# Kernel tuning notes

Measured on AMD Instinct MI355X. Metric: run time of the kernel, lower is better.

Reference implementation:

```python
import jax, jax.numpy as jnp
import numpy as np
import math

N = 100000   # nodes
E = 1600000  # edges
D = 128      # embed_dim
H = 8        # nhead
HD = D // H  # head dim
EPS = 1e-16  # matches torch_geometric-style segment softmax eps


def _xavier(key, shape):
    fan_out, fan_in = shape
    lim = math.sqrt(6.0 / (fan_in + fan_out))
    return jax.random.uniform(key, shape, jnp.float32, -lim, lim)


def setup_inputs() -> dict:
    key = jax.random.key(0)
    ks = jax.random.split(key, 8)
    return {
        "feats": jax.random.normal(ks[0], (N, D), jnp.float32),
        "edge_index": jax.random.randint(ks[1], (E, 2), 0, N, dtype=jnp.int64),
        "edge_attr": jax.random.normal(ks[2], (E, 1), jnp.float32),
        "Wq": _xavier(ks[3], (D, D)), "bq": jnp.zeros((D,), jnp.float32),
        "Wk": _xavier(ks[4], (D, D)), "bk": jnp.zeros((D,), jnp.float32),
        "Wv": _xavier(ks[5], (D, D)), "bv": jnp.zeros((D,), jnp.float32),
        "Wo": _xavier(ks[6], (D, D)), "bo": jnp.zeros((D,), jnp.float32),
    }


def reference(feats, edge_index, edge_attr, Wq, bq, Wk, bk, Wv, bv, Wo, bo):
    # feats: [N, D]; edge_index: [E, 2] with r=src, c=dst; edge_attr unused (mult_attr=0)
    n = feats.shape[0]
    q = (feats @ Wq.T + bq).reshape(n, H, HD)  # [N, H, hd]
    k = (feats @ Wk.T + bk).reshape(n, H, HD)
    v = (feats @ Wv.T + bv).reshape(n, H, HD)

    r = edge_index[:, 0]
    c = edge_index[:, 1]

    # per-edge dot-product scores: q[dst] . k[src]
    scores = jnp.einsum('ehd,ehd->eh', q[c], k[r]) / math.sqrt(HD)  # [E, H]

    # segment softmax over edges grouped by destination node c
    smax = jax.ops.segment_max(scores, c, num_segments=n)  # [N, H]
    ex = jnp.exp(scores - smax[c])
    ssum = jax.ops.segment_sum(ex, c, num_segments=n)      # [N, H]
    alpha = ex / (ssum[c] + EPS)                           # [E, H]
    # (dropout is identity at eval time; mult_attr=0 so edge_attr unused)

    # weighted scatter-aggregate of values into destination nodes
    out = jax.ops.segment_sum(alpha[:, :, None] * v[r], c, num_segments=n)  # [N, H, hd]
    out = out.reshape(n, D) @ Wo.T + bo
    return out
```

## Files before the change

### kernel.cpp

```cpp
#include <hip/hip_runtime.h>
#include <hip/hip_bf16.h>

typedef __attribute__((ext_vector_type(8))) short bh8;
typedef __attribute__((ext_vector_type(4))) float f32x4;

__device__ __forceinline__ float bfbits2f(unsigned short s) {
    union { unsigned int u; float f; } cv;
    cv.u = ((unsigned int)s) << 16;
    return cv.f;
}
__device__ __forceinline__ unsigned short f2bfbits(float f) {
    union { float f; unsigned int u; } cv; cv.f = f;
    unsigned int u = cv.u;
    u += 0x7fffu + ((u >> 16) & 1u);
    return (unsigned short)(u >> 16);
}
__device__ __forceinline__ unsigned int pack2bf(float a, float b) {
    return (unsigned int)f2bfbits(a) | (((unsigned int)f2bfbits(b)) << 16);
}

__device__ __forceinline__ bh8 load_frag_f32(const float* __restrict__ p) {
    float4 f0 = *reinterpret_cast<const float4*>(p);
    float4 f1 = *reinterpret_cast<const float4*>(p + 4);
    bh8 r;
    r[0] = (short)f2bfbits(f0.x); r[1] = (short)f2bfbits(f0.y);
    r[2] = (short)f2bfbits(f0.z); r[3] = (short)f2bfbits(f0.w);
    r[4] = (short)f2bfbits(f1.x); r[5] = (short)f2bfbits(f1.y);
    r[6] = (short)f2bfbits(f1.z); r[7] = (short)f2bfbits(f1.w);
    return r;
}

__global__ __launch_bounds__(256)
void wconv_kernel(const float* __restrict__ w0, const float* __restrict__ w1,
                  const float* __restrict__ w2, const float* __restrict__ w3,
                  unsigned short* __restrict__ o0, unsigned short* __restrict__ o1,
                  unsigned short* __restrict__ o2, unsigned short* __restrict__ o3)
{
    const float* src[4] = {w0, w1, w2, w3};
    unsigned short* dst[4] = {o0, o1, o2, o3};
    const float* s = src[blockIdx.y];
    unsigned short* d = dst[blockIdx.y];
    int i = (blockIdx.x * 256 + threadIdx.x) * 4;
    float4 f = *reinterpret_cast<const float4*>(&s[i]);
    uint2 p;
    p.x = pack2bf(f.x, f.y);
    p.y = pack2bf(f.z, f.w);
    *reinterpret_cast<uint2*>(&d[i]) = p;
}

__global__ __launch_bounds__(256)
void qkv_scatter(const float* __restrict__ A,
                 const unsigned short* __restrict__ Wqb, const float* __restrict__ bq,
                 const unsigned short* __restrict__ Wkb, const float* __restrict__ bk,
                 const unsigned short* __restrict__ Wvb, const float* __restrict__ bv,
                 unsigned short* __restrict__ Oq, unsigned short* __restrict__ Ok,
                 unsigned short* __restrict__ Ov, int M, int gx,
                 const int* __restrict__ ei, const int* __restrict__ offsets,
                 const int* __restrict__ rank, int* __restrict__ sorted_r,
                 int E, int nsb)
{
    if (blockIdx.x >= (unsigned)gx) {
        int sb = blockIdx.x - gx;
        int stride = nsb * 256;
        for (int e = sb * 256 + threadIdx.x; e < E; e += stride) {
            int2 rc = reinterpret_cast<const int2*>(ei)[e];
            sorted_r[offsets[rc.y] + rank[e]] = rc.x;
        }
        return;
    }

    const int lane = threadIdx.x & 63;
    const int w    = threadIdx.x >> 6;
    const int r0   = blockIdx.x * 128 + w * 32;
    const int lr   = lane & 15;
    const int lk   = (lane >> 4) * 8;
    const int cq   = (lane >> 4) * 4;

    bh8 a[2][4];
    #pragma unroll
    for (int jt = 0; jt < 2; jt++) {
        int row = r0 + jt * 16 + lr; if (row >= M) row = M - 1;
        const float* ap = &A[(size_t)row * 128 + lk];
        #pragma unroll
        for (int ks = 0; ks < 4; ks++) a[jt][ks] = load_frag_f32(ap + ks * 32);
    }

    const unsigned short* Ws[3] = {Wqb, Wkb, Wvb};
    const float* Bs[3] = {bq, bk, bv};
    unsigned short* Os[3] = {Oq, Ok, Ov};

    #pragma unroll
    for (int wsel = 0; wsel < 3; wsel++) {
        const unsigned short* W = Ws[wsel];
        f32x4 acc[2][8];
        #pragma unroll
        for (int jt = 0; jt < 2; jt++)
            #pragma unroll
            for (int it = 0; it < 8; it++)
                #pragma unroll
                for (int q = 0; q < 4; q++) acc[jt][it][q] = 0.f;

        #pragma unroll
        for (int ks = 0; ks < 4; ks++) {
            bh8 b[8];
            #pragma unroll
            for (int it = 0; it < 8; it++)
                b[it] = *reinterpret_cast<const bh8*>(
                    &W[(size_t)(it * 16 + lr) * 128 + ks * 32 + lk]);
            #pragma unroll
            for (int jt = 0; jt < 2; jt++)
                #pragma unroll
                for (int it = 0; it < 8; it++)
                    acc[jt][it] = __builtin_amdgcn_mfma_f32_16x16x32_bf16(
                        b[it], a[jt][ks], acc[jt][it], 0, 0, 0);
        }

        const float* bias = Bs[wsel];
        unsigned short* O = Os[wsel];
        #pragma unroll
        for (int jt = 0; jt < 2; jt++) {
            int row = r0 + jt * 16 + lr;
            if (row >= M) continue;
            #pragma unroll
            for (int it = 0; it < 8; it++) {
                float4 b4 = *reinterpret_cast<const float4*>(&bias[it * 16 + cq]);
                uint2 pk;
                pk.x = pack2bf(acc[jt][it][0] + b4.x, acc[jt][it][1] + b4.y);
                pk.y = pack2bf(acc[jt][it][2] + b4.z, acc[jt][it][3] + b4.w);
                *reinterpret_cast<uint2*>(&O[(size_t)row * 128 + it * 16 + cq]) = pk;
            }
        }
    }
}

__global__ __launch_bounds__(256)
void out_gemm(const unsigned short* __restrict__ A, const unsigned short* __restrict__ Wb,
              const float* __restrict__ bias, float* __restrict__ O, int M)
{
    const int lane = threadIdx.x & 63;
    const int w    = threadIdx.x >> 6;
    const int r0   = blockIdx.x * 128 + w * 32;
    const int lr   = lane & 15;
    const int lk   = (lane >> 4) * 8;
    const int cq   = (lane >> 4) * 4;

    bh8 a[2][4];
    #pragma unroll
    for (int jt = 0; jt < 2; jt++) {
        int row = r0 + jt * 16 + lr; if (row >= M) row = M - 1;
        const unsigned short* ap = &A[(size_t)row * 128 + lk];
        #pragma unroll
        for (int ks = 0; ks < 4; ks++)
            a[jt][ks] = *reinterpret_cast<const bh8*>(ap + ks * 32);
    }

    f32x4 acc[2][8];
    #pragma unroll
    for (int jt = 0; jt < 2; jt++)
        #pragma unroll
        for (int it = 0; it < 8; it++)
            #pragma unroll
            for (int q = 0; q < 4; q++) acc[jt][it][q] = 0.f;

    #pragma unroll
    for (int ks = 0; ks < 4; ks++) {
        bh8 b[8];
        #pragma unroll
        for (int it = 0; it < 8; it++)
            b[it] = *reinterpret_cast<const bh8*>(
                &Wb[(size_t)(it * 16 + lr) * 128 + ks * 32 + lk]);
        #pragma unroll
        for (int jt = 0; jt < 2; jt++)
            #pragma unroll
            for (int it = 0; it < 8; it++)
                acc[jt][it] = __builtin_amdgcn_mfma_f32_16x16x32_bf16(
                    b[it], a[jt][ks], acc[jt][it], 0, 0, 0);
    }

    #pragma unroll
    for (int jt = 0; jt < 2; jt++) {
        int row = r0 + jt * 16 + lr;
        if (row >= M) continue;
        #pragma unroll
        for (int it = 0; it < 8; it++) {
            float4 b4 = *reinterpret_cast<const float4*>(&bias[it * 16 + cq]);
            float4 o;
            o.x = acc[jt][it][0] + b4.x;
            o.y = acc[jt][it][1] + b4.y;
            o.z = acc[jt][it][2] + b4.z;
            o.w = acc[jt][it][3] + b4.w;
            *reinterpret_cast<float4*>(&O[(size_t)row * 128 + it * 16 + cq]) = o;
        }
    }
}

__global__ void hist_kernel(const int* __restrict__ ei, int* __restrict__ counts,
                            int* __restrict__ rank, int E)
{
    int e = blockIdx.x * blockDim.x + threadIdx.x;
    if (e < E) {
        int2 rc = reinterpret_cast<const int2*>(ei)[e];
        rank[e] = atomicAdd(&counts[rc.y], 1);
    }
}

__device__ __forceinline__ int wave_incl_scan(int v, int lane) {
    #pragma unroll
    for (int off = 1; off < 64; off <<= 1) {
        int y = __shfl_up(v, off);
        if (lane >= off) v += y;
    }
    return v;
}

__global__ __launch_bounds__(1024)
void scan1_kernel(const int* __restrict__ counts, int* __restrict__ offs,
                  int* __restrict__ blkSum, int n)
{
    __shared__ int wsum[16];
    __shared__ int woff[16];
    const int t = threadIdx.x, lane = t & 63, w = t >> 6;
    int i = blockIdx.x * 1024 + t;
    int x = (i < n) ? counts[i] : 0;
    int v = wave_incl_scan(x, lane);
    if (lane == 63) wsum[w] = v;
    __syncthreads();
    if (t == 0) {
        int s = 0;
        #pragma unroll
        for (int j = 0; j < 16; j++) { int tmp = wsum[j]; woff[j] = s; s += tmp; }
        blkSum[blockIdx.x] = s;
    }
    __syncthreads();
    if (i < n) offs[i] = woff[w] + v - x;
}

__global__ void scan2_kernel(const int* __restrict__ blkSum, int* __restrict__ blkOff,
                             int* __restrict__ offs, int nb, int n)
{
    const int lane = threadIdx.x;
    int carry = 0;
    for (int base = 0; base < nb; base += 64) {
        int x = (base + lane < nb) ? blkSum[base + lane] : 0;
        int v = wave_incl_scan(x, lane);
        if (base + lane < nb) blkOff[base + lane] = carry + v - x;
        carry += __shfl(v, 63);
    }
    if (lane == 0) offs[n] = carry;
}

__global__ __launch_bounds__(1024)
void scan3_kernel(int* __restrict__ offs, const int* __restrict__ blkOff, int n)
{
    int i = blockIdx.x * 1024 + threadIdx.x;
    if (i < n) offs[i] += blkOff[blockIdx.x];
}

__global__ __launch_bounds__(256)
void edge_attn_kernel(const unsigned short* __restrict__ qb,
                      const unsigned short* __restrict__ kb,
                      const unsigned short* __restrict__ vb,
                      const int* __restrict__ offsets,
                      const int* __restrict__ sorted_r,
                      unsigned short* __restrict__ acc_out, int n)
{
    const int lane = threadIdx.x & 63;
    const int wid  = threadIdx.x >> 6;
    const int node = blockIdx.x * 4 + wid;
    if (node >= n) return;

    const int h    = lane & 7;
    const int eloc = lane >> 3;
    const int seg0 = __builtin_amdgcn_readfirstlane(offsets[node]);
    const int segL = __builtin_amdgcn_readfirstlane(offsets[node + 1]) - seg0;
    const int nch  = (segL + 7) >> 3;
    const int* __restrict__ sr = sorted_r + seg0;

    float qf[16];
    {
        const uint4* p = reinterpret_cast<const uint4*>(&qb[(size_t)node * 128 + h * 16]);
        uint4 u0 = p[0], u1 = p[1];
        unsigned int uu[8] = {u0.x, u0.y, u0.z, u0.w, u1.x, u1.y, u1.z, u1.w};
        #pragma unroll
        for (int i = 0; i < 8; i++) {
            qf[2 * i]     = bfbits2f((unsigned short)(uu[i] & 0xffffu));
            qf[2 * i + 1] = bfbits2f((unsigned short)(uu[i] >> 16));
        }
    }

    float acc0 = 0.f, acc1 = 0.f, ssum = 0.f;

    uint4 kA0, kA1, kB0, kB1;
    unsigned int vA[8], vB[8];

    if (nch > 0) {
        int idx = (eloc < segL) ? eloc : (segL - 1);
        int rk  = sr[idx];
        const uint4* kp = reinterpret_cast<const uint4*>(&kb[(size_t)rk * 128 + h * 16]);
        kA0 = kp[0]; kA1 = kp[1];
        int ec0 = (segL < 8) ? segL : 8;
        #pragma unroll
        for (int e = 0; e < 8; e++) {
            int re = sr[(e < ec0) ? e : (ec0 - 1)];
            vA[e] = *reinterpret_cast<const unsigned int*>(&vb[(size_t)re * 128 + 2 * lane]);
        }
    }

    auto step = [&](int c, const uint4& ck0, const uint4& ck1, const unsigned int (&cv)[8],
                    uint4& nk0, uint4& nk1, unsigned int (&nv)[8]) {
        const int base = c << 3;
        if (c + 1 < nch) {
            int nb   = base + 8;
            int nidx = nb + eloc;
            int rk   = sr[(nidx < segL) ? nidx : (segL - 1)];
            const uint4* kp = reinterpret_cast<const uint4*>(&kb[(size_t)rk * 128 + h * 16]);
            nk0 = kp[0]; nk1 = kp[1];
            int ecn = segL - nb; if (ecn > 8) ecn = 8;
            #pragma unroll
            for (int e = 0; e < 8; e++) {
                int re = sr[nb + ((e < ecn) ? e : (ecn - 1))];
                nv[e] = *reinterpret_cast<const unsigned int*>(&vb[(size_t)re * 128 + 2 * lane]);
            }
        }
        unsigned int uu[8] = {ck0.x, ck0.y, ck0.z, ck0.w, ck1.x, ck1.y, ck1.z, ck1.w};
        float s = 0.f;
        #pragma unroll
        for (int i = 0; i < 8; i++) {
            s += qf[2 * i]     * bfbits2f((unsigned short)(uu[i] & 0xffffu));
            s += qf[2 * i + 1] * bfbits2f((unsigned short)(uu[i] >> 16));
        }
        float ex = (base + eloc < segL) ? __expf(s * 0.25f) : 0.f;
        ssum += ex;
        #pragma unroll
        for (int e = 0; e < 8; e++) {
            float exv = __shfl(ex, e * 8 + eloc);
            acc0 += exv * bfbits2f((unsigned short)(cv[e] & 0xffffu));
            acc1 += exv * bfbits2f((unsigned short)(cv[e] >> 16));
        }
    };

    int c = 0;
    while (c < nch) {
        step(c, kA0, kA1, vA, kB0, kB1, vB); c++;
        if (c >= nch) break;
        step(c, kB0, kB1, vB, kA0, kA1, vA); c++;
    }

    ssum += __shfl_xor(ssum, 8);
    ssum += __shfl_xor(ssum, 16);
    ssum += __shfl_xor(ssum, 32);
    float den = __shfl(ssum, lane >> 3) + 1e-16f;
    float rd  = 1.0f / den;

    reinterpret_cast<unsigned int*>(acc_out)[(size_t)node * 64 + lane] =
        pack2bf(acc0 * rd, acc1 * rd);
}

extern "C" void kernel_launch(void* const* d_in, const int* in_sizes, int n_in,
                              void* d_out, int out_size, void* d_ws, size_t ws_size,
                              hipStream_t stream)
{
    const float* feats = (const float*)d_in[0];
    const int*   ei    = (const int*)d_in[1];
    const float* Wq = (const float*)d_in[3];
    const float* bq = (const float*)d_in[4];
    const float* Wk = (const float*)d_in[5];
    const float* bk = (const float*)d_in[6];
    const float* Wv = (const float*)d_in[7];
    const float* bv = (const float*)d_in[8];
    const float* Wo = (const float*)d_in[9];
    const float* bo = (const float*)d_in[10];
    float* out = (float*)d_out;

    const int N = in_sizes[0] / 128;
    const int E = in_sizes[1] / 2;
    const int nb = (N + 1023) / 1024;

    char* ws = (char*)d_ws;
    size_t off = 0;
    auto alloc = [&](size_t bytes) -> void* {
        void* p = ws + off;
        off += (bytes + 255) & ~(size_t)255;
        return p;
    };
    unsigned short* qb   = (unsigned short*)alloc((size_t)N * 128 * 2);
    unsigned short* kb   = (unsigned short*)alloc((size_t)N * 128 * 2);
    unsigned short* vb   = (unsigned short*)alloc((size_t)N * 128 * 2);
    unsigned short* accb = (unsigned short*)alloc((size_t)N * 128 * 2);
    int* rank     = (int*)accb;
    int* counts   = (int*)alloc(((size_t)N + 1) * 4);
    int* offsets  = (int*)alloc(((size_t)N + 1) * 4);
    int* sorted_r = (int*)alloc((size_t)E * 4);
    int* blkSum   = (int*)alloc(256 * 4);
    int* blkOff   = (int*)alloc(256 * 4);
    unsigned short* Wqb = (unsigned short*)alloc(128 * 128 * 2);
    unsigned short* Wkb = (unsigned short*)alloc(128 * 128 * 2);
    unsigned short* Wvb = (unsigned short*)alloc(128 * 128 * 2);
    unsigned short* Wob = (unsigned short*)alloc(128 * 128 * 2);

    hipMemsetAsync(counts, 0, ((size_t)N + 1) * 4, stream);

    wconv_kernel<<<dim3(16, 4), 256, 0, stream>>>(Wq, Wk, Wv, Wo, Wqb, Wkb, Wvb, Wob);

    hist_kernel<<<(E + 255) / 256, 256, 0, stream>>>(ei, counts, rank, E);
    scan1_kernel<<<nb, 1024, 0, stream>>>(counts, offsets, blkSum, N);
    scan2_kernel<<<1, 64, 0, stream>>>(blkSum, blkOff, offsets, nb, N);
    scan3_kernel<<<nb, 1024, 0, stream>>>(offsets, blkOff, N);

    const int gx  = (N + 127) / 128;
    const int nsb = 1024;
    qkv_scatter<<<gx + nsb, 256, 0, stream>>>(feats, Wqb, bq, Wkb, bk, Wvb, bv,
                                              qb, kb, vb, N, gx,
                                              ei, offsets, rank, sorted_r, E, nsb);

    edge_attn_kernel<<<(N + 3) / 4, 256, 0, stream>>>(qb, kb, vb, offsets, sorted_r, accb, N);

    out_gemm<<<gx, 256, 0, stream>>>(accb, Wob, bo, out, N);
}
```

Baseline: 302.6 us.

## Replace rank-based edge scatter with two-pass bucketed counting sort

The CSR build no longer records a per-edge rank with global atomics. Edges are first binned into coarse buckets of 256 destination nodes, using shared-memory histograms and one global atomic per bucket per 4096-edge chunk. A new fine_scatter kernel then places each bucket's edges into sorted_r with per-node atomics, so the random writes stay within a small region. The weight conversion is also fused into the histogram kernel launch. In exchange the change adds an extra kernel and an intermediate int2 edge buffer pass, and the within-node edge order becomes nondeterministic, as before.

```diff
diff --git a/kernel.cpp b/kernel.cpp
--- a/kernel.cpp
+++ b/kernel.cpp
@@ -3,6 +3,9 @@
 
 typedef __attribute__((ext_vector_type(8))) short bh8;
 typedef __attribute__((ext_vector_type(4))) float f32x4;
+
+#define BUCKET_SHIFT 8
+#define MAXBUCKETS 1024
 
 __device__ __forceinline__ float bfbits2f(unsigned short s) {
     union { unsigned int u; float f; } cv;
@@ -31,176 +34,29 @@
 }
 
 __global__ __launch_bounds__(256)
-void wconv_kernel(const float* __restrict__ w0, const float* __restrict__ w1,
-                  const float* __restrict__ w2, const float* __restrict__ w3,
-                  unsigned short* __restrict__ o0, unsigned short* __restrict__ o1,
-                  unsigned short* __restrict__ o2, unsigned short* __restrict__ o3)
-{
-    const float* src[4] = {w0, w1, w2, w3};
-    unsigned short* dst[4] = {o0, o1, o2, o3};
-    const float* s = src[blockIdx.y];
-    unsigned short* d = dst[blockIdx.y];
-    int i = (blockIdx.x * 256 + threadIdx.x) * 4;
-    float4 f = *reinterpret_cast<const float4*>(&s[i]);
-    uint2 p;
-    p.x = pack2bf(f.x, f.y);
-    p.y = pack2bf(f.z, f.w);
-    *reinterpret_cast<uint2*>(&d[i]) = p;
-}
-
-__global__ __launch_bounds__(256)
-void qkv_scatter(const float* __restrict__ A,
-                 const unsigned short* __restrict__ Wqb, const float* __restrict__ bq,
-                 const unsigned short* __restrict__ Wkb, const float* __restrict__ bk,
-                 const unsigned short* __restrict__ Wvb, const float* __restrict__ bv,
-                 unsigned short* __restrict__ Oq, unsigned short* __restrict__ Ok,
-                 unsigned short* __restrict__ Ov, int M, int gx,
-                 const int* __restrict__ ei, const int* __restrict__ offsets,
-                 const int* __restrict__ rank, int* __restrict__ sorted_r,
-                 int E, int nsb)
-{
-    if (blockIdx.x >= (unsigned)gx) {
-        int sb = blockIdx.x - gx;
-        int stride = nsb * 256;
-        for (int e = sb * 256 + threadIdx.x; e < E; e += stride) {
-            int2 rc = reinterpret_cast<const int2*>(ei)[e];
-            sorted_r[offsets[rc.y] + rank[e]] = rc.x;
-        }
+void wconv_hist(const float* __restrict__ w0, const float* __restrict__ w1,
+                const float* __restrict__ w2, const float* __restrict__ w3,
+                unsigned short* __restrict__ o0, unsigned short* __restrict__ o1,
+                unsigned short* __restrict__ o2, unsigned short* __restrict__ o3,
+                const int* __restrict__ ei, int* __restrict__ counts, int E)
+{
+    if (blockIdx.x < 64) {
+        const float* src[4] = {w0, w1, w2, w3};
+        unsigned short* dst[4] = {o0, o1, o2, o3};
+        const float* s = src[blockIdx.x >> 4];
+        unsigned short* d = dst[blockIdx.x >> 4];
+        int i = ((blockIdx.x & 15) * 256 + threadIdx.x) * 4;
+        float4 f = *reinterpret_cast<const float4*>(&s[i]);
+        uint2 p;
+        p.x = pack2bf(f.x, f.y);
+        p.y = pack2bf(f.z, f.w);
+        *reinterpret_cast<uint2*>(&d[i]) = p;
         return;
     }
-
-    const int lane = threadIdx.x & 63;
-    const int w    = threadIdx.x >> 6;
-    const int r0   = blockIdx.x * 128 + w * 32;
-    const int lr   = lane & 15;
-    const int lk   = (lane >> 4) * 8;
-    const int cq   = (lane >> 4) * 4;
-
-    bh8 a[2][4];
-    #pragma unroll
-    for (int jt = 0; jt < 2; jt++) {
-        int row = r0 + jt * 16 + lr; if (row >= M) row = M - 1;
-        const float* ap = &A[(size_t)row * 128 + lk];
-        #pragma unroll
-        for (int ks = 0; ks < 4; ks++) a[jt][ks] = load_frag_f32(ap + ks * 32);
-    }
-
-    const unsigned short* Ws[3] = {Wqb, Wkb, Wvb};
-    const float* Bs[3] = {bq, bk, bv};
-    unsigned short* Os[3] = {Oq, Ok, Ov};
-
-    #pragma unroll
-    for (int wsel = 0; wsel < 3; wsel++) {
-        const unsigned short* W = Ws[wsel];
-        f32x4 acc[2][8];
-        #pragma unroll
-        for (int jt = 0; jt < 2; jt++)
-            #pragma unroll
-            for (int it = 0; it < 8; it++)
-                #pragma unroll
-                for (int q = 0; q < 4; q++) acc[jt][it][q] = 0.f;
-
-        #pragma unroll
-        for (int ks = 0; ks < 4; ks++) {
-            bh8 b[8];
-            #pragma unroll
-            for (int it = 0; it < 8; it++)
-                b[it] = *reinterpret_cast<const bh8*>(
-                    &W[(size_t)(it * 16 + lr) * 128 + ks * 32 + lk]);
-            #pragma unroll
-            for (int jt = 0; jt < 2; jt++)
-                #pragma unroll
-                for (int it = 0; it < 8; it++)
-                    acc[jt][it] = __builtin_amdgcn_mfma_f32_16x16x32_bf16(
-                        b[it], a[jt][ks], acc[jt][it], 0, 0, 0);
-        }
-
-        const float* bias = Bs[wsel];
-        unsigned short* O = Os[wsel];
-        #pragma unroll
-        for (int jt = 0; jt < 2; jt++) {
-            int row = r0 + jt * 16 + lr;
-            if (row >= M) continue;
-            #pragma unroll
-            for (int it = 0; it < 8; it++) {
-                float4 b4 = *reinterpret_cast<const float4*>(&bias[it * 16 + cq]);
-                uint2 pk;
-                pk.x = pack2bf(acc[jt][it][0] + b4.x, acc[jt][it][1] + b4.y);
-                pk.y = pack2bf(acc[jt][it][2] + b4.z, acc[jt][it][3] + b4.w);
-                *reinterpret_cast<uint2*>(&O[(size_t)row * 128 + it * 16 + cq]) = pk;
-            }
-        }
-    }
-}
-
-__global__ __launch_bounds__(256)
-void out_gemm(const unsigned short* __restrict__ A, const unsigned short* __restrict__ Wb,
-              const float* __restrict__ bias, float* __restrict__ O, int M)
-{
-    const int lane = threadIdx.x & 63;
-    const int w    = threadIdx.x >> 6;
-    const int r0   = blockIdx.x * 128 + w * 32;
-    const int lr   = lane & 15;
-    const int lk   = (lane >> 4) * 8;
-    const int cq   = (lane >> 4) * 4;
-
-    bh8 a[2][4];
-    #pragma unroll
-    for (int jt = 0; jt < 2; jt++) {
-        int row = r0 + jt * 16 + lr; if (row >= M) row = M - 1;
-        const unsigned short* ap = &A[(size_t)row * 128 + lk];
-        #pragma unroll
-        for (int ks = 0; ks < 4; ks++)
-            a[jt][ks] = *reinterpret_cast<const bh8*>(ap + ks * 32);
-    }
-
-    f32x4 acc[2][8];
-    #pragma unroll
-    for (int jt = 0; jt < 2; jt++)
-        #pragma unroll
-        for (int it = 0; it < 8; it++)
-            #pragma unroll
-            for (int q = 0; q < 4; q++) acc[jt][it][q] = 0.f;
-
-    #pragma unroll
-    for (int ks = 0; ks < 4; ks++) {
-        bh8 b[8];
-        #pragma unroll
-        for (int it = 0; it < 8; it++)
-            b[it] = *reinterpret_cast<const bh8*>(
-                &Wb[(size_t)(it * 16 + lr) * 128 + ks * 32 + lk]);
-        #pragma unroll
-        for (int jt = 0; jt < 2; jt++)
-            #pragma unroll
-            for (int it = 0; it < 8; it++)
-                acc[jt][it] = __builtin_amdgcn_mfma_f32_16x16x32_bf16(
-                    b[it], a[jt][ks], acc[jt][it], 0, 0, 0);
-    }
-
-    #pragma unroll
-    for (int jt = 0; jt < 2; jt++) {
-        int row = r0 + jt * 16 + lr;
-        if (row >= M) continue;
-        #pragma unroll
-        for (int it = 0; it < 8; it++) {
-            float4 b4 = *reinterpret_cast<const float4*>(&bias[it * 16 + cq]);
-            float4 o;
-            o.x = acc[jt][it][0] + b4.x;
-            o.y = acc[jt][it][1] + b4.y;
-            o.z = acc[jt][it][2] + b4.z;
-            o.w = acc[jt][it][3] + b4.w;
-            *reinterpret_cast<float4*>(&O[(size_t)row * 128 + it * 16 + cq]) = o;
-        }
-    }
-}
-
-__global__ void hist_kernel(const int* __restrict__ ei, int* __restrict__ counts,
-                            int* __restrict__ rank, int E)
-{
-    int e = blockIdx.x * blockDim.x + threadIdx.x;
+    int e = (blockIdx.x - 64) * 256 + threadIdx.x;
     if (e < E) {
         int2 rc = reinterpret_cast<const int2*>(ei)[e];
-        rank[e] = atomicAdd(&counts[rc.y], 1);
+        atomicAdd(&counts[rc.y], 1);
     }
 }
 
@@ -257,6 +113,132 @@
 }
 
 __global__ __launch_bounds__(256)
+void qkv_binscatter(const float* __restrict__ A,
+                    const unsigned short* __restrict__ Wqb, const float* __restrict__ bq,
+                    const unsigned short* __restrict__ Wkb, const float* __restrict__ bk,
+                    const unsigned short* __restrict__ Wvb, const float* __restrict__ bv,
+                    unsigned short* __restrict__ Oq, unsigned short* __restrict__ Ok,
+                    unsigned short* __restrict__ Ov, int M, int gx,
+                    const int* __restrict__ ei, const int* __restrict__ offsets,
+                    int* __restrict__ bfill, int2* __restrict__ ebuf,
+                    int E, int nsb)
+{
+    __shared__ int hcnt[MAXBUCKETS];
+    __shared__ int hbase[MAXBUCKETS];
+
+    if (blockIdx.x >= (unsigned)gx) {
+        const int nbuckets = (M + (1 << BUCKET_SHIFT) - 1) >> BUCKET_SHIFT;
+        const int sb = blockIdx.x - gx;
+        for (int chunk0 = sb * 4096; chunk0 < E; chunk0 += nsb * 4096) {
+            for (int i = threadIdx.x; i < nbuckets; i += 256) hcnt[i] = 0;
+            __syncthreads();
+            int2 ed[16]; int lrk[16];
+            #pragma unroll
+            for (int j = 0; j < 16; j++) {
+                int e = chunk0 + j * 256 + threadIdx.x;
+                if (e < E) {
+                    ed[j] = reinterpret_cast<const int2*>(ei)[e];
+                    lrk[j] = atomicAdd(&hcnt[ed[j].y >> BUCKET_SHIFT], 1);
+                }
+            }
+            __syncthreads();
+            for (int b = threadIdx.x; b < nbuckets; b += 256) {
+                int cnt = hcnt[b];
+                int gb = cnt ? atomicAdd(&bfill[b], cnt) : 0;
+                hbase[b] = offsets[b << BUCKET_SHIFT] + gb;
+            }
+            __syncthreads();
+            #pragma unroll
+            for (int j = 0; j < 16; j++) {
+                int e = chunk0 + j * 256 + threadIdx.x;
+                if (e < E)
+                    ebuf[hbase[ed[j].y >> BUCKET_SHIFT] + lrk[j]] = ed[j];
+            }
+            __syncthreads();
+        }
+        return;
+    }
+
+    const int lane = threadIdx.x & 63;
+    const int w    = threadIdx.x >> 6;
+    const int r0   = blockIdx.x * 128 + w * 32;
+    const int lr   = lane & 15;
+    const int lk   = (lane >> 4) * 8;
+    const int cq   = (lane >> 4) * 4;
+
+    bh8 a[2][4];
+    #pragma unroll
+    for (int jt = 0; jt < 2; jt++) {
+        int row = r0 + jt * 16 + lr; if (row >= M) row = M - 1;
+        const float* ap = &A[(size_t)row * 128 + lk];
+        #pragma unroll
+        for (int ks = 0; ks < 4; ks++) a[jt][ks] = load_frag_f32(ap + ks * 32);
+    }
+
+    const unsigned short* Ws[3] = {Wqb, Wkb, Wvb};
+    const float* Bs[3] = {bq, bk, bv};
+    unsigned short* Os[3] = {Oq, Ok, Ov};
+
+    #pragma unroll
+    for (int wsel = 0; wsel < 3; wsel++) {
+        const unsigned short* W = Ws[wsel];
+        f32x4 acc[2][8];
+        #pragma unroll
+        for (int jt = 0; jt < 2; jt++)
+            #pragma unroll
+            for (int it = 0; it < 8; it++)
+                #pragma unroll
+                for (int q = 0; q < 4; q++) acc[jt][it][q] = 0.f;
+
+        #pragma unroll
+        for (int ks = 0; ks < 4; ks++) {
+            bh8 b[8];
+            #pragma unroll
+            for (int it = 0; it < 8; it++)
+                b[it] = *reinterpret_cast<const bh8*>(
+                    &W[(size_t)(it * 16 + lr) * 128 + ks * 32 + lk]);
+            #pragma unroll
+            for (int jt = 0; jt < 2; jt++)
+                #pragma unroll
+                for (int it = 0; it < 8; it++)
+                    acc[jt][it] = __builtin_amdgcn_mfma_f32_16x16x32_bf16(
+                        b[it], a[jt][ks], acc[jt][it], 0, 0, 0);
+        }
+
+        const float* bias = Bs[wsel];
+        unsigned short* O = Os[wsel];
+        #pragma unroll
+        for (int jt = 0; jt < 2; jt++) {
+            int row = r0 + jt * 16 + lr;
+            if (row >= M) continue;
+            #pragma unroll
+            for (int it = 0; it < 8; it++) {
+                float4 b4 = *reinterpret_cast<const float4*>(&bias[it * 16 + cq]);
+                uint2 pk;
+                pk.x = pack2bf(acc[jt][it][0] + b4.x, acc[jt][it][1] + b4.y);
+                pk.y = pack2bf(acc[jt][it][2] + b4.z, acc[jt][it][3] + b4.w);
+                *reinterpret_cast<uint2*>(&O[(size_t)row * 128 + it * 16 + cq]) = pk;
+            }
+        }
+    }
+}
+
+__global__ __launch_bounds__(256)
+void fine_scatter(const int2* __restrict__ ebuf, const int* __restrict__ offsets,
+                  int* __restrict__ fill2, int* __restrict__ sorted_r, int N)
+{
+    int nb0 = blockIdx.x << BUCKET_SHIFT;
+    int lo = offsets[nb0];
+    int hi_idx = nb0 + (1 << BUCKET_SHIFT);
+    int hi = offsets[hi_idx > N ? N : hi_idx];
+    for (int i = lo + threadIdx.x; i < hi; i += 256) {
+        int2 rc = ebuf[i];
+        int pos = offsets[rc.y] + atomicAdd(&fill2[rc.y], 1);
+        sorted_r[pos] = rc.x;
+    }
+}
+
+__global__ __launch_bounds__(256)
 void edge_attn_kernel(const unsigned short* __restrict__ qb,
                       const unsigned short* __restrict__ kb,
                       const unsigned short* __restrict__ vb,
@@ -354,6 +336,67 @@
 
     reinterpret_cast<unsigned int*>(acc_out)[(size_t)node * 64 + lane] =
         pack2bf(acc0 * rd, acc1 * rd);
+}
+
+__global__ __launch_bounds__(256)
+void out_gemm(const unsigned short* __restrict__ A, const unsigned short* __restrict__ Wb,
+              const float* __restrict__ bias, float* __restrict__ O, int M)
+{
+    const int lane = threadIdx.x & 63;
+    const int w    = threadIdx.x >> 6;
+    const int r0   = blockIdx.x * 128 + w * 32;
+    const int lr   = lane & 15;
+    const int lk   = (lane >> 4) * 8;
+    const int cq   = (lane >> 4) * 4;
+
+    bh8 a[2][4];
+    #pragma unroll
+    for (int jt = 0; jt < 2; jt++) {
+        int row = r0 + jt * 16 + lr; if (row >= M) row = M - 1;
+        const unsigned short* ap = &A[(size_t)row * 128 + lk];
+        #pragma unroll
+        for (int ks = 0; ks < 4; ks++)
+            a[jt][ks] = *reinterpret_cast<const bh8*>(ap + ks * 32);
+    }
+
+    f32x4 acc[2][8];
+    #pragma unroll
+    for (int jt = 0; jt < 2; jt++)
+        #pragma unroll
+        for (int it = 0; it < 8; it++)
+            #pragma unroll
+            for (int q = 0; q < 4; q++) acc[jt][it][q] = 0.f;
+
+    #pragma unroll
+    for (int ks = 0; ks < 4; ks++) {
+        bh8 b[8];
+        #pragma unroll
+        for (int it = 0; it < 8; it++)
+            b[it] = *reinterpret_cast<const bh8*>(
+                &Wb[(size_t)(it * 16 + lr) * 128 + ks * 32 + lk]);
+        #pragma unroll
+        for (int jt = 0; jt < 2; jt++)
+            #pragma unroll
+            for (int it = 0; it < 8; it++)
+                acc[jt][it] = __builtin_amdgcn_mfma_f32_16x16x32_bf16(
+                    b[it], a[jt][ks], acc[jt][it], 0, 0, 0);
+    }
+
+    #pragma unroll
+    for (int jt = 0; jt < 2; jt++) {
+        int row = r0 + jt * 16 + lr;
+        if (row >= M) continue;
+        #pragma unroll
+        for (int it = 0; it < 8; it++) {
+            float4 b4 = *reinterpret_cast<const float4*>(&bias[it * 16 + cq]);
+            float4 o;
+            o.x = acc[jt][it][0] + b4.x;
+            o.y = acc[jt][it][1] + b4.y;
+            o.z = acc[jt][it][2] + b4.z;
+            o.w = acc[jt][it][3] + b4.w;
+            *reinterpret_cast<float4*>(&O[(size_t)row * 128 + it * 16 + cq]) = o;
+        }
+    }
 }
 
 extern "C" void kernel_launch(void* const* d_in, const int* in_sizes, int n_in,
@@ -375,6 +418,7 @@
     const int N = in_sizes[0] / 128;
     const int E = in_sizes[1] / 2;
     const int nb = (N + 1023) / 1024;
+    const int nbuckets = (N + (1 << BUCKET_SHIFT) - 1) >> BUCKET_SHIFT;
 
     char* ws = (char*)d_ws;
     size_t off = 0;
@@ -387,8 +431,10 @@
     unsigned short* kb   = (unsigned short*)alloc((size_t)N * 128 * 2);
     unsigned short* vb   = (unsigned short*)alloc((size_t)N * 128 * 2);
     unsigned short* accb = (unsigned short*)alloc((size_t)N * 128 * 2);
-    int* rank     = (int*)accb;
-    int* counts   = (int*)alloc(((size_t)N + 1) * 4);
+    int2* ebuf    = (int2*)accb;
+    int* counts   = (int*)alloc(((size_t)N + 1 + N + MAXBUCKETS) * 4);
+    int* fill2    = counts + (N + 1);
+    int* bfill    = fill2 + N;
     int* offsets  = (int*)alloc(((size_t)N + 1) * 4);
     int* sorted_r = (int*)alloc((size_t)E * 4);
     int* blkSum   = (int*)alloc(256 * 4);
@@ -398,20 +444,22 @@
     unsigned short* Wvb = (unsigned short*)alloc(128 * 128 * 2);
     unsigned short* Wob = (unsigned short*)alloc(128 * 128 * 2);
 
-    hipMemsetAsync(counts, 0, ((size_t)N + 1) * 4, stream);
-
-    wconv_kernel<<<dim3(16, 4), 256, 0, stream>>>(Wq, Wk, Wv, Wo, Wqb, Wkb, Wvb, Wob);
-
-    hist_kernel<<<(E + 255) / 256, 256, 0, stream>>>(ei, counts, rank, E);
+    hipMemsetAsync(counts, 0, ((size_t)N + 1 + N + MAXBUCKETS) * 4, stream);
+
+    wconv_hist<<<64 + (E + 255) / 256, 256, 0, stream>>>(
+        Wq, Wk, Wv, Wo, Wqb, Wkb, Wvb, Wob, ei, counts, E);
+
     scan1_kernel<<<nb, 1024, 0, stream>>>(counts, offsets, blkSum, N);
     scan2_kernel<<<1, 64, 0, stream>>>(blkSum, blkOff, offsets, nb, N);
     scan3_kernel<<<nb, 1024, 0, stream>>>(offsets, blkOff, N);
 
     const int gx  = (N + 127) / 128;
-    const int nsb = 1024;
-    qkv_scatter<<<gx + nsb, 256, 0, stream>>>(feats, Wqb, bq, Wkb, bk, Wvb, bv,
-                                              qb, kb, vb, N, gx,
-                                              ei, offsets, rank, sorted_r, E, nsb);
+    const int nsb = (E + 4095) / 4096;
+    qkv_binscatter<<<gx + nsb, 256, 0, stream>>>(feats, Wqb, bq, Wkb, bk, Wvb, bv,
+                                                 qb, kb, vb, N, gx,
+                                                 ei, offsets, bfill, ebuf, E, nsb);
+
+    fine_scatter<<<nbuckets, 256, 0, stream>>>(ebuf, offsets, fill2, sorted_r, N);
 
     edge_attn_kernel<<<(N + 3) / 4, 256, 0, stream>>>(qb, kb, vb, offsets, sorted_r, accb, N);
 
```

Measured after the change: 331.2 us. 1.09x slower.

## Process 16 edges per chunk in edge attention and fuse weight conversion with histogram

Applied to the files above, without the earlier changes.

The edge attention kernel now gives each lane two heads' 32-wide slices of q/k and handles 16 edges per chunk instead of 8. This halves the number of serial chunk iterations per node and loads more K/V rows in flight. The weight bf16 conversion and the destination histogram are merged into one launch to save a kernel launch. The cost is higher register pressure from 16-entry V buffers and 8 uint4 K registers, which may lower occupancy, plus extra wasted lanes for nodes with few edges.

```diff
diff --git a/kernel.cpp b/kernel.cpp
--- a/kernel.cpp
+++ b/kernel.cpp
@@ -17,6 +17,14 @@
 }
 __device__ __forceinline__ unsigned int pack2bf(float a, float b) {
     return (unsigned int)f2bfbits(a) | (((unsigned int)f2bfbits(b)) << 16);
+}
+__device__ __forceinline__ void unpack8(const uint4& u, float* f) {
+    unsigned int uu[4] = {u.x, u.y, u.z, u.w};
+    #pragma unroll
+    for (int i = 0; i < 4; i++) {
+        f[2 * i]     = bfbits2f((unsigned short)(uu[i] & 0xffffu));
+        f[2 * i + 1] = bfbits2f((unsigned short)(uu[i] >> 16));
+    }
 }
 
 __device__ __forceinline__ bh8 load_frag_f32(const float* __restrict__ p) {
@@ -31,21 +39,83 @@
 }
 
 __global__ __launch_bounds__(256)
-void wconv_kernel(const float* __restrict__ w0, const float* __restrict__ w1,
-                  const float* __restrict__ w2, const float* __restrict__ w3,
-                  unsigned short* __restrict__ o0, unsigned short* __restrict__ o1,
-                  unsigned short* __restrict__ o2, unsigned short* __restrict__ o3)
-{
-    const float* src[4] = {w0, w1, w2, w3};
-    unsigned short* dst[4] = {o0, o1, o2, o3};
-    const float* s = src[blockIdx.y];
-    unsigned short* d = dst[blockIdx.y];
-    int i = (blockIdx.x * 256 + threadIdx.x) * 4;
-    float4 f = *reinterpret_cast<const float4*>(&s[i]);
-    uint2 p;
-    p.x = pack2bf(f.x, f.y);
-    p.y = pack2bf(f.z, f.w);
-    *reinterpret_cast<uint2*>(&d[i]) = p;
+void wconv_hist(const float* __restrict__ w0, const float* __restrict__ w1,
+                const float* __restrict__ w2, const float* __restrict__ w3,
+                unsigned short* __restrict__ o0, unsigned short* __restrict__ o1,
+                unsigned short* __restrict__ o2, unsigned short* __restrict__ o3,
+                const int* __restrict__ ei, int* __restrict__ counts,
+                int* __restrict__ rank, int E)
+{
+    if (blockIdx.x < 64) {
+        const float* src[4] = {w0, w1, w2, w3};
+        unsigned short* dst[4] = {o0, o1, o2, o3};
+        const float* s = src[blockIdx.x >> 4];
+        unsigned short* d = dst[blockIdx.x >> 4];
+        int i = ((blockIdx.x & 15) * 256 + threadIdx.x) * 4;
+        float4 f = *reinterpret_cast<const float4*>(&s[i]);
+        uint2 p;
+        p.x = pack2bf(f.x, f.y);
+        p.y = pack2bf(f.z, f.w);
+        *reinterpret_cast<uint2*>(&d[i]) = p;
+        return;
+    }
+    int e = (blockIdx.x - 64) * 256 + threadIdx.x;
+    if (e < E) {
+        int2 rc = reinterpret_cast<const int2*>(ei)[e];
+        rank[e] = atomicAdd(&counts[rc.y], 1);
+    }
+}
+
+__device__ __forceinline__ int wave_incl_scan(int v, int lane) {
+    #pragma unroll
+    for (int off = 1; off < 64; off <<= 1) {
+        int y = __shfl_up(v, off);
+        if (lane >= off) v += y;
+    }
+    return v;
+}
+
+__global__ __launch_bounds__(1024)
+void scan1_kernel(const int* __restrict__ counts, int* __restrict__ offs,
+                  int* __restrict__ blkSum, int n)
+{
+    __shared__ int wsum[16];
+    __shared__ int woff[16];
+    const int t = threadIdx.x, lane = t & 63, w = t >> 6;
+    int i = blockIdx.x * 1024 + t;
+    int x = (i < n) ? counts[i] : 0;
+    int v = wave_incl_scan(x, lane);
+    if (lane == 63) wsum[w] = v;
+    __syncthreads();
+    if (t == 0) {
+        int s = 0;
+        #pragma unroll
+        for (int j = 0; j < 16; j++) { int tmp = wsum[j]; woff[j] = s; s += tmp; }
+        blkSum[blockIdx.x] = s;
+    }
+    __syncthreads();
+    if (i < n) offs[i] = woff[w] + v - x;
+}
+
+__global__ void scan2_kernel(const int* __restrict__ blkSum, int* __restrict__ blkOff,
+                             int* __restrict__ offs, int nb, int n)
+{
+    const int lane = threadIdx.x;
+    int carry = 0;
+    for (int base = 0; base < nb; base += 64) {
+        int x = (base + lane < nb) ? blkSum[base + lane] : 0;
+        int v = wave_incl_scan(x, lane);
+        if (base + lane < nb) blkOff[base + lane] = carry + v - x;
+        carry += __shfl(v, 63);
+    }
+    if (lane == 0) offs[n] = carry;
+}
+
+__global__ __launch_bounds__(1024)
+void scan3_kernel(int* __restrict__ offs, const int* __restrict__ blkOff, int n)
+{
+    int i = blockIdx.x * 1024 + threadIdx.x;
+    if (i < n) offs[i] += blkOff[blockIdx.x];
 }
 
 __global__ __launch_bounds__(256)
@@ -134,6 +204,121 @@
 }
 
 __global__ __launch_bounds__(256)
+void edge_attn_kernel(const unsigned short* __restrict__ qb,
+                      const unsigned short* __restrict__ kb,
+                      const unsigned short* __restrict__ vb,
+                      const int* __restrict__ offsets,
+                      const int* __restrict__ sorted_r,
+                      unsigned short* __restrict__ acc_out, int n)
+{
+    const int lane = threadIdx.x & 63;
+    const int wid  = threadIdx.x >> 6;
+    const int node = blockIdx.x * 4 + wid;
+    if (node >= n) return;
+
+    const int s    = lane >> 2;
+    const int sub  = lane & 3;
+    const int hp   = lane >> 4;
+    const int hsel = (lane >> 3) & 1;
+    const int seg0 = __builtin_amdgcn_readfirstlane(offsets[node]);
+    const int segL = __builtin_amdgcn_readfirstlane(offsets[node + 1]) - seg0;
+    const int nch  = (segL + 15) >> 4;
+    const int* __restrict__ sr = sorted_r + seg0;
+
+    float qA[16], qB[16];
+    {
+        const uint4* p = reinterpret_cast<const uint4*>(&qb[(size_t)node * 128 + sub * 32]);
+        uint4 u0 = p[0], u1 = p[1], u2 = p[2], u3 = p[3];
+        unpack8(u0, qA); unpack8(u1, qA + 8);
+        unpack8(u2, qB); unpack8(u3, qB + 8);
+    }
+
+    float acc0 = 0.f, acc1 = 0.f, ssumA = 0.f, ssumB = 0.f;
+
+    uint4 kA0, kA1, kA2, kA3, kB0, kB1, kB2, kB3;
+    unsigned int vA[16], vB[16];
+
+    if (nch > 0) {
+        int idx = (s < segL) ? s : (segL - 1);
+        int rk  = sr[idx];
+        const uint4* kp = reinterpret_cast<const uint4*>(&kb[(size_t)rk * 128 + sub * 32]);
+        kA0 = kp[0]; kA1 = kp[1]; kA2 = kp[2]; kA3 = kp[3];
+        int ec0 = (segL < 16) ? segL : 16;
+        #pragma unroll
+        for (int e = 0; e < 16; e++) {
+            int re = sr[(e < ec0) ? e : (ec0 - 1)];
+            vA[e] = *reinterpret_cast<const unsigned int*>(&vb[(size_t)re * 128 + 2 * lane]);
+        }
+    }
+
+    auto step = [&](int c,
+                    const uint4& ck0, const uint4& ck1, const uint4& ck2, const uint4& ck3,
+                    const unsigned int (&cv)[16],
+                    uint4& nk0, uint4& nk1, uint4& nk2, uint4& nk3,
+                    unsigned int (&nv)[16]) {
+        const int base = c << 4;
+        if (c + 1 < nch) {
+            int nb   = base + 16;
+            int nidx = nb + s;
+            int rk   = sr[(nidx < segL) ? nidx : (segL - 1)];
+            const uint4* kp = reinterpret_cast<const uint4*>(&kb[(size_t)rk * 128 + sub * 32]);
+            nk0 = kp[0]; nk1 = kp[1]; nk2 = kp[2]; nk3 = kp[3];
+            int ecn = segL - nb; if (ecn > 16) ecn = 16;
+            #pragma unroll
+            for (int e = 0; e < 16; e++) {
+                int re = sr[nb + ((e < ecn) ? e : (ecn - 1))];
+                nv[e] = *reinterpret_cast<const unsigned int*>(&vb[(size_t)re * 128 + 2 * lane]);
+            }
+        }
+        float kf[8];
+        float sAv = 0.f, sBv = 0.f;
+        unpack8(ck0, kf);
+        #pragma unroll
+        for (int i = 0; i < 8; i++) sAv += qA[i] * kf[i];
+        unpack8(ck1, kf);
+        #pragma unroll
+        for (int i = 0; i < 8; i++) sAv += qA[8 + i] * kf[i];
+        unpack8(ck2, kf);
+        #pragma unroll
+        for (int i = 0; i < 8; i++) sBv += qB[i] * kf[i];
+        unpack8(ck3, kf);
+        #pragma unroll
+        for (int i = 0; i < 8; i++) sBv += qB[8 + i] * kf[i];
+        bool valid = (base + s) < segL;
+        float exA = valid ? __expf(sAv * 0.25f) : 0.f;
+        float exB = valid ? __expf(sBv * 0.25f) : 0.f;
+        ssumA += exA; ssumB += exB;
+        #pragma unroll
+        for (int e = 0; e < 16; e++) {
+            float eA = __shfl(exA, e * 4 + hp);
+            float eB = __shfl(exB, e * 4 + hp);
+            float exv = hsel ? eB : eA;
+            acc0 += exv * bfbits2f((unsigned short)(cv[e] & 0xffffu));
+            acc1 += exv * bfbits2f((unsigned short)(cv[e] >> 16));
+        }
+    };
+
+    int c = 0;
+    while (c < nch) {
+        step(c, kA0, kA1, kA2, kA3, vA, kB0, kB1, kB2, kB3, vB); c++;
+        if (c >= nch) break;
+        step(c, kB0, kB1, kB2, kB3, vB, kA0, kA1, kA2, kA3, vA); c++;
+    }
+
+    ssumA += __shfl_xor(ssumA, 4);  ssumB += __shfl_xor(ssumB, 4);
+    ssumA += __shfl_xor(ssumA, 8);  ssumB += __shfl_xor(ssumB, 8);
+    ssumA += __shfl_xor(ssumA, 16); ssumB += __shfl_xor(ssumB, 16);
+    ssumA += __shfl_xor(ssumA, 32); ssumB += __shfl_xor(ssumB, 32);
+    float denA = __shfl(ssumA, hp);
+    float denB = __shfl(ssumB, hp);
+    float den  = (hsel ? denB : denA) + 1e-16f;
+    float rd   = 1.0f / den;
+
+    reinterpret_cast<unsigned int*>(acc_out)[(size_t)node * 64 + lane] =
+        pack2bf(acc0 * rd, acc1 * rd);
+}
+
+__global__ __launch_bounds__(256)
 void out_gemm(const unsigned short* __restrict__ A, const unsigned short* __restrict__ Wb,
               const float* __restrict__ bias, float* __restrict__ O, int M)
 {
@@ -192,168 +377,6 @@
             *reinterpret_cast<float4*>(&O[(size_t)row * 128 + it * 16 + cq]) = o;
         }
     }
-}
-
-__global__ void hist_kernel(const int* __restrict__ ei, int* __restrict__ counts,
-                            int* __restrict__ rank, int E)
-{
-    int e = blockIdx.x * blockDim.x + threadIdx.x;
-    if (e < E) {
-        int2 rc = reinterpret_cast<const int2*>(ei)[e];
-        rank[e] = atomicAdd(&counts[rc.y], 1);
-    }
-}
-
-__device__ __forceinline__ int wave_incl_scan(int v, int lane) {
-    #pragma unroll
-    for (int off = 1; off < 64; off <<= 1) {
-        int y = __shfl_up(v, off);
-        if (lane >= off) v += y;
-    }
-    return v;
-}
-
-__global__ __launch_bounds__(1024)
-void scan1_kernel(const int* __restrict__ counts, int* __restrict__ offs,
-                  int* __restrict__ blkSum, int n)
-{
-    __shared__ int wsum[16];
-    __shared__ int woff[16];
-    const int t = threadIdx.x, lane = t & 63, w = t >> 6;
-    int i = blockIdx.x * 1024 + t;
-    int x = (i < n) ? counts[i] : 0;
-    int v = wave_incl_scan(x, lane);
-    if (lane == 63) wsum[w] = v;
-    __syncthreads();
-    if (t == 0) {
-        int s = 0;
-        #pragma unroll
-        for (int j = 0; j < 16; j++) { int tmp = wsum[j]; woff[j] = s; s += tmp; }
-        blkSum[blockIdx.x] = s;
-    }
-    __syncthreads();
-    if (i < n) offs[i] = woff[w] + v - x;
-}
-
-__global__ void scan2_kernel(const int* __restrict__ blkSum, int* __restrict__ blkOff,
-                             int* __restrict__ offs, int nb, int n)
-{
-    const int lane = threadIdx.x;
-    int carry = 0;
-    for (int base = 0; base < nb; base += 64) {
-        int x = (base + lane < nb) ? blkSum[base + lane] : 0;
-        int v = wave_incl_scan(x, lane);
-        if (base + lane < nb) blkOff[base + lane] = carry + v - x;
-        carry += __shfl(v, 63);
-    }
-    if (lane == 0) offs[n] = carry;
-}
-
-__global__ __launch_bounds__(1024)
-void scan3_kernel(int* __restrict__ offs, const int* __restrict__ blkOff, int n)
-{
-    int i = blockIdx.x * 1024 + threadIdx.x;
-    if (i < n) offs[i] += blkOff[blockIdx.x];
-}
-
-__global__ __launch_bounds__(256)
-void edge_attn_kernel(const unsigned short* __restrict__ qb,
-                      const unsigned short* __restrict__ kb,
-                      const unsigned short* __restrict__ vb,
-                      const int* __restrict__ offsets,
-                      const int* __restrict__ sorted_r,
-                      unsigned short* __restrict__ acc_out, int n)
-{
-    const int lane = threadIdx.x & 63;
-    const int wid  = threadIdx.x >> 6;
-    const int node = blockIdx.x * 4 + wid;
-    if (node >= n) return;
-
-    const int h    = lane & 7;
-    const int eloc = lane >> 3;
-    const int seg0 = __builtin_amdgcn_readfirstlane(offsets[node]);
-    const int segL = __builtin_amdgcn_readfirstlane(offsets[node + 1]) - seg0;
-    const int nch  = (segL + 7) >> 3;
-    const int* __restrict__ sr = sorted_r + seg0;
-
-    float qf[16];
-    {
-        const uint4* p = reinterpret_cast<const uint4*>(&qb[(size_t)node * 128 + h * 16]);
-        uint4 u0 = p[0], u1 = p[1];
-        unsigned int uu[8] = {u0.x, u0.y, u0.z, u0.w, u1.x, u1.y, u1.z, u1.w};
-        #pragma unroll
-        for (int i = 0; i < 8; i++) {
-            qf[2 * i]     = bfbits2f((unsigned short)(uu[i] & 0xffffu));
-            qf[2 * i + 1] = bfbits2f((unsigned short)(uu[i] >> 16));
-        }
-    }
-
-    float acc0 = 0.f, acc1 = 0.f, ssum = 0.f;
-
-    uint4 kA0, kA1, kB0, kB1;
-    unsigned int vA[8], vB[8];
-
-    if (nch > 0) {
-        int idx = (eloc < segL) ? eloc : (segL - 1);
-        int rk  = sr[idx];
-        const uint4* kp = reinterpret_cast<const uint4*>(&kb[(size_t)rk * 128 + h * 16]);
-        kA0 = kp[0]; kA1 = kp[1];
-        int ec0 = (segL < 8) ? segL : 8;
-        #pragma unroll
-        for (int e = 0; e < 8; e++) {
-            int re = sr[(e < ec0) ? e : (ec0 - 1)];
-            vA[e] = *reinterpret_cast<const unsigned int*>(&vb[(size_t)re * 128 + 2 * lane]);
-        }
-    }
-
-    auto step = [&](int c, const uint4& ck0, const uint4& ck1, const unsigned int (&cv)[8],
-                    uint4& nk0, uint4& nk1, unsigned int (&nv)[8]) {
-        const int base = c << 3;
-        if (c + 1 < nch) {
-            int nb   = base + 8;
-            int nidx = nb + eloc;
-            int rk   = sr[(nidx < segL) ? nidx : (segL - 1)];
-            const uint4* kp = reinterpret_cast<const uint4*>(&kb[(size_t)rk * 128 + h * 16]);
-            nk0 = kp[0]; nk1 = kp[1];
-            int ecn = segL - nb; if (ecn > 8) ecn = 8;
-            #pragma unroll
-            for (int e = 0; e < 8; e++) {
-                int re = sr[nb + ((e < ecn) ? e : (ecn - 1))];
-                nv[e] = *reinterpret_cast<const unsigned int*>(&vb[(size_t)re * 128 + 2 * lane]);
-            }
-        }
-        unsigned int uu[8] = {ck0.x, ck0.y, ck0.z, ck0.w, ck1.x, ck1.y, ck1.z, ck1.w};
-        float s = 0.f;
-        #pragma unroll
-        for (int i = 0; i < 8; i++) {
-            s += qf[2 * i]     * bfbits2f((unsigned short)(uu[i] & 0xffffu));
-            s += qf[2 * i + 1] * bfbits2f((unsigned short)(uu[i] >> 16));
-        }
-        float ex = (base + eloc < segL) ? __expf(s * 0.25f) : 0.f;
-        ssum += ex;
-        #pragma unroll
-        for (int e = 0; e < 8; e++) {
-            float exv = __shfl(ex, e * 8 + eloc);
-            acc0 += exv * bfbits2f((unsigned short)(cv[e] & 0xffffu));
-            acc1 += exv * bfbits2f((unsigned short)(cv[e] >> 16));
-        }
-    };
-
-    int c = 0;
-    while (c < nch) {
-        step(c, kA0, kA1, vA, kB0, kB1, vB); c++;
-        if (c >= nch) break;
-        step(c, kB0, kB1, vB, kA0, kA1, vA); c++;
-    }
-
-    ssum += __shfl_xor(ssum, 8);
-    ssum += __shfl_xor(ssum, 16);
-    ssum += __shfl_xor(ssum, 32);
-    float den = __shfl(ssum, lane >> 3) + 1e-16f;
-    float rd  = 1.0f / den;
-
-    reinterpret_cast<unsigned int*>(acc_out)[(size_t)node * 64 + lane] =
-        pack2bf(acc0 * rd, acc1 * rd);
 }
 
 extern "C" void kernel_launch(void* const* d_in, const int* in_sizes, int n_in,
@@ -400,9 +423,9 @@
 
     hipMemsetAsync(counts, 0, ((size_t)N + 1) * 4, stream);
 
-    wconv_kernel<<<dim3(16, 4), 256, 0, stream>>>(Wq, Wk, Wv, Wo, Wqb, Wkb, Wvb, Wob);
-
-    hist_kernel<<<(E + 255) / 256, 256, 0, stream>>>(ei, counts, rank, E);
+    wconv_hist<<<64 + (E + 255) / 256, 256, 0, stream>>>(
+        Wq, Wk, Wv, Wo, Wqb, Wkb, Wvb, Wob, ei, counts, rank, E);
+
     scan1_kernel<<<nb, 1024, 0, stream>>>(counts, offsets, blkSum, N);
     scan2_kernel<<<1, 64, 0, stream>>>(blkSum, blkOff, offsets, nb, N);
     scan3_kernel<<<nb, 1024, 0, stream>>>(offsets, blkOff, N);
```

Result: slower. 339.5 us (+12.2%).
